# Kernel optimization log

Measured on AMD Instinct MI355X. Metric: run time of the kernel, lower is better.

## Reference

```python
import jax, jax.numpy as jnp
import numpy as np

B, D1, D2 = 131072, 40, 10   # batch, features, timesteps
T0, T1 = 120, 5              # template[1]
O0, O1 = 3, 1                # output_dim


def setup_inputs() -> dict:
    key = jax.random.key(0)
    ks = jax.random.split(key, 7)
    s = 0.1
    return {
        "x": jax.random.normal(ks[0], (B, D1, D2), dtype=jnp.float32),
        "W11": jax.random.normal(ks[1], (T0, D1), dtype=jnp.float32) * s,
        "fc2_w": jax.random.normal(ks[2], (T1, D2), dtype=jnp.float32) * s,  # nn.Linear(D2,T1) weight
        "bias1": jax.random.normal(ks[3], (T0, T1), dtype=jnp.float32) * s,
        "W12": jax.random.normal(ks[4], (O0, T0), dtype=jnp.float32) * s,
        "fc4_w": jax.random.normal(ks[5], (O1, T1), dtype=jnp.float32) * s,  # nn.Linear(T1,O1) weight
        "bias2": jax.random.normal(ks[6], (O0, O1), dtype=jnp.float32) * s,
    }


def reference(x, W11, fc2_w, bias1, W12, fc4_w, bias2):
    # item1[b] = W11 @ x[b]                 -> [B, T0, D2]
    item1 = jnp.einsum("td,bds->bts", W11, x)
    # item2[b] = fc2(item1[b]) + bias1      -> [B, T0, T1]; dropout is identity at eval
    item2 = jax.nn.relu(jnp.einsum("bts,us->btu", item1, fc2_w) + bias1)
    # item3[b] = W12 @ item2[b]             -> [B, O0, T1]
    item3 = jnp.einsum("ot,btu->bou", W12, item2)
    # item4[b] = fc4(item3[b]) + bias2      -> [B, O0, O1]
    item4 = jnp.einsum("bou,pu->bop", item3, fc4_w) + bias2
    # output_dim[1] == 1 -> squeeze last dim -> [B, O0]
    return item4[..., 0]
```

## Files before the change

### kernel.cpp

```cpp
#include <hip/hip_runtime.h>

#define NB  131072
#define ND1 40
#define ND2 10
#define NT0 120
#define NT1 5
#define NO0 3

#define NBW 32
#define XTILE (NBW * ND1 * ND2)
#define PK  40

typedef __attribute__((ext_vector_type(8))) short  short8;
typedef __attribute__((ext_vector_type(4))) float  f32x4;

static __device__ __forceinline__ unsigned short f2bf(float f) {
    union { float f; unsigned u; } v; v.f = f;
    unsigned r = v.u + 0x7FFFu + ((v.u >> 16) & 1u);
    return (unsigned short)(r >> 16);
}

__global__ __launch_bounds__(256, 2) void BL_36721970381090_kernel(
    const float* __restrict__ x,
    const float* __restrict__ W11,
    const float* __restrict__ fc2_w,
    const float* __restrict__ bias1,
    const float* __restrict__ W12,
    const float* __restrict__ fc4_w,
    const float* __restrict__ bias2,
    float* __restrict__ out)
{
    __shared__ __align__(16) unsigned short Ybf[NT1 * NBW * PK];
    __shared__ float biasL[128 * NT1];
    __shared__ float w12L[NO0 * 128];
    __shared__ float b2L[4];
    __shared__ float redL[4 * NO0 * NBW];

    const int tid = threadIdx.x;
    const int wg  = blockIdx.x;
    const int w   = tid >> 6;
    const int l   = tid & 63;
    const int lr  = l & 15;
    const int lg  = l >> 4;

    for (int i = tid; i < 128 * NT1; i += 256)
        biasL[i] = (i < NT0 * NT1) ? bias1[i] : 0.f;
    for (int i = tid; i < NO0 * 128; i += 256) {
        const int o = i >> 7, t = i & 127;
        w12L[i] = (t < NT0) ? W12[o * NT0 + t] : 0.f;
    }
    if (tid < NO0) b2L[tid] = bias2[tid];

    float fc4r[NT1];
#pragma unroll
    for (int u = 0; u < NT1; ++u) fc4r[u] = fc4_w[u];

    short8 afr[2][2];
#pragma unroll
    for (int mt = 0; mt < 2; ++mt) {
        const int t  = w * 32 + mt * 16 + lr;
        const int tc = t < NT0 ? t : NT0 - 1;
#pragma unroll
        for (int kk = 0; kk < 2; ++kk) {
            const int cb = kk * 32 + lg * 8;
            const int cc = cb <= 32 ? cb : 0;
            const float4* pw = (const float4*)(W11 + tc * ND1 + cc);
            const float4 w0 = pw[0], w1 = pw[1];
            const bool v = (t < NT0) && (cb <= 32);
            short8 f;
            f[0] = v ? (short)f2bf(w0.x) : (short)0;
            f[1] = v ? (short)f2bf(w0.y) : (short)0;
            f[2] = v ? (short)f2bf(w0.z) : (short)0;
            f[3] = v ? (short)f2bf(w0.w) : (short)0;
            f[4] = v ? (short)f2bf(w1.x) : (short)0;
            f[5] = v ? (short)f2bf(w1.y) : (short)0;
            f[6] = v ? (short)f2bf(w1.z) : (short)0;
            f[7] = v ? (short)f2bf(w1.w) : (short)0;
            afr[mt][kk] = f;
        }
    }

    {
        const float* gx = x + (size_t)wg * XTILE;
        unsigned* Yw = (unsigned*)Ybf;
#pragma unroll
        for (int rep = 0; rep < 3; ++rep) {
            const int  q   = rep * 256 + tid;
            const bool act = (rep < 2) || (tid < 128);
            if (act) {
                const int batch = q / 20;
                const int pair  = q - batch * 20;
                float4 xq[5];
                const float4* xr = (const float4*)(gx + q * 20);
#pragma unroll
                for (int i = 0; i < 5; ++i) xq[i] = xr[i];
                const float* xv = (const float*)xq;
#pragma unroll
                for (int u = 0; u < NT1; ++u) {
                    float a0 = 0.f, a1 = 0.f;
#pragma unroll
                    for (int s = 0; s < ND2; ++s) {
                        const float fw = fc2_w[u * ND2 + s];
                        a0 = fmaf(xv[s], fw, a0);
                        a1 = fmaf(xv[10 + s], fw, a1);
                    }
                    Yw[u * (NBW * PK / 2) + batch * (PK / 2) + pair] =
                        (unsigned)f2bf(a0) | ((unsigned)f2bf(a1) << 16);
                }
            }
        }
    }
    __syncthreads();

    float st[2][2][4];
#pragma unroll
    for (int mt = 0; mt < 2; ++mt)
#pragma unroll
        for (int nt = 0; nt < 2; ++nt)
#pragma unroll
            for (int r = 0; r < 4; ++r) st[mt][nt][r] = 0.f;

    const short8 zf = {0, 0, 0, 0, 0, 0, 0, 0};
#pragma unroll
    for (int u = 0; u < NT1; ++u) {
        float bv[2][4];
#pragma unroll
        for (int mt = 0; mt < 2; ++mt)
#pragma unroll
            for (int r = 0; r < 4; ++r)
                bv[mt][r] = biasL[(w * 32 + mt * 16 + lg * 4 + r) * NT1 + u];
        const unsigned short* Yu = &Ybf[u * (NBW * PK)];
#pragma unroll
        for (int nt = 0; nt < 2; ++nt) {
            const short8 b0 = *(const short8*)&Yu[(nt * 16 + lr) * PK + lg * 8];
            short8 b1 = zf;
            if (lg == 0) b1 = *(const short8*)&Yu[(nt * 16 + lr) * PK + 32];
#pragma unroll
            for (int mt = 0; mt < 2; ++mt) {
                f32x4 z = {0.f, 0.f, 0.f, 0.f};
                z = __builtin_amdgcn_mfma_f32_16x16x32_bf16(afr[mt][0], b0, z, 0, 0, 0);
                z = __builtin_amdgcn_mfma_f32_16x16x32_bf16(afr[mt][1], b1, z, 0, 0, 0);
#pragma unroll
                for (int r = 0; r < 4; ++r)
                    st[mt][nt][r] += fc4r[u] * fmaxf(z[r] + bv[mt][r], 0.f);
            }
        }
    }

    float po[2][NO0];
#pragma unroll
    for (int nt = 0; nt < 2; ++nt)
#pragma unroll
        for (int o = 0; o < NO0; ++o) {
            float a = 0.f;
#pragma unroll
            for (int mt = 0; mt < 2; ++mt)
#pragma unroll
                for (int r = 0; r < 4; ++r)
                    a = fmaf(w12L[o * 128 + (w * 32 + mt * 16 + lg * 4 + r)],
                             st[mt][nt][r], a);
            a += __shfl_xor(a, 16, 64);
            a += __shfl_xor(a, 32, 64);
            po[nt][o] = a;
        }
    if (l < 16) {
#pragma unroll
        for (int nt = 0; nt < 2; ++nt)
#pragma unroll
            for (int o = 0; o < NO0; ++o)
                redL[(w * NO0 + o) * NBW + nt * 16 + l] = po[nt][o];
    }
    __syncthreads();

    if (tid < NO0 * NBW) {
        const int o  = tid >> 5;
        const int bc = tid & 31;
        const float s = redL[(0 * NO0 + o) * NBW + bc]
                      + redL[(1 * NO0 + o) * NBW + bc]
                      + redL[(2 * NO0 + o) * NBW + bc]
                      + redL[(3 * NO0 + o) * NBW + bc]
                      + b2L[o];
        out[((size_t)wg * NBW + bc) * NO0 + o] = s;
    }
}

extern "C" void kernel_launch(void* const* d_in, const int* in_sizes, int n_in,
                              void* d_out, int out_size, void* d_ws, size_t ws_size,
                              hipStream_t stream) {
    const float* x      = (const float*)d_in[0];
    const float* W11    = (const float*)d_in[1];
    const float* fc2_w  = (const float*)d_in[2];
    const float* bias1  = (const float*)d_in[3];
    const float* W12    = (const float*)d_in[4];
    const float* fc4_w  = (const float*)d_in[5];
    const float* bias2  = (const float*)d_in[6];
    float* out = (float*)d_out;

    const int blocks = NB / NBW;
    BL_36721970381090_kernel<<<blocks, 256, 0, stream>>>(
        x, W11, fc2_w, bias1, W12, fc4_w, bias2, out);
}
```

Measured before the change: 50.71 us.

## Process two batch tiles per workgroup with software-pipelined load and compute

```diff
diff --git a/kernel.cpp b/kernel.cpp
--- a/kernel.cpp
+++ b/kernel.cpp
@@ -8,7 +8,7 @@
 #define NO0 3
 
 #define NBW 32
-#define XTILE (NBW * ND1 * ND2)
+#define XT  (NBW * ND1 * ND2)
 #define PK  40
 
 typedef __attribute__((ext_vector_type(8))) short  short8;
@@ -20,7 +20,7 @@
     return (unsigned short)(r >> 16);
 }
 
-__global__ __launch_bounds__(256, 2) void BL_36721970381090_kernel(
+__global__ __launch_bounds__(256) void BL_36721970381090_kernel(
     const float* __restrict__ x,
     const float* __restrict__ W11,
     const float* __restrict__ fc2_w,
@@ -30,11 +30,13 @@
     const float* __restrict__ bias2,
     float* __restrict__ out)
 {
-    __shared__ __align__(16) unsigned short Ybf[NT1 * NBW * PK];
+    __shared__ __align__(16) unsigned short YbfA[NT1 * NBW * PK];
+    __shared__ __align__(16) unsigned short YbfB[NT1 * NBW * PK];
     __shared__ float biasL[128 * NT1];
     __shared__ float w12L[NO0 * 128];
     __shared__ float b2L[4];
-    __shared__ float redL[4 * NO0 * NBW];
+    __shared__ float redLA[4 * NO0 * NBW];
+    __shared__ float redLB[4 * NO0 * NBW];
 
     const int tid = threadIdx.x;
     const int wg  = blockIdx.x;
@@ -80,21 +82,29 @@
         }
     }
 
-    {
-        const float* gx = x + (size_t)wg * XTILE;
-        unsigned* Yw = (unsigned*)Ybf;
+    const float* gxA = x + (size_t)(2 * wg) * XT;
+    const float* gxB = gxA + XT;
+
+    auto LOADX = [&](const float* gx, float4 (&xq)[3][5]) {
 #pragma unroll
         for (int rep = 0; rep < 3; ++rep) {
-            const int  q   = rep * 256 + tid;
-            const bool act = (rep < 2) || (tid < 128);
-            if (act) {
+            if (rep < 2 || tid < 128) {
+                const int q = rep * 256 + tid;
+                const float4* xr = (const float4*)(gx + q * 20);
+#pragma unroll
+                for (int i = 0; i < 5; ++i) xq[rep][i] = xr[i];
+            }
+        }
+    };
+    auto COMPY = [&](const float4 (&xq)[3][5], unsigned short* Yb) {
+        unsigned* Yw = (unsigned*)Yb;
+#pragma unroll
+        for (int rep = 0; rep < 3; ++rep) {
+            if (rep < 2 || tid < 128) {
+                const int q = rep * 256 + tid;
                 const int batch = q / 20;
                 const int pair  = q - batch * 20;
-                float4 xq[5];
-                const float4* xr = (const float4*)(gx + q * 20);
-#pragma unroll
-                for (int i = 0; i < 5; ++i) xq[i] = xr[i];
-                const float* xv = (const float*)xq;
+                const float* xv = (const float*)&xq[rep][0];
 #pragma unroll
                 for (int u = 0; u < NT1; ++u) {
                     float a0 = 0.f, a1 = 0.f;
@@ -109,79 +119,105 @@
                 }
             }
         }
-    }
-    __syncthreads();
-
-    float st[2][2][4];
-#pragma unroll
-    for (int mt = 0; mt < 2; ++mt)
+    };
+    auto PHASE2 = [&](const unsigned short* Yb, float (&po)[2][NO0]) {
+        float st[2][2][4];
+#pragma unroll
+        for (int mt = 0; mt < 2; ++mt)
+#pragma unroll
+            for (int nt = 0; nt < 2; ++nt)
+#pragma unroll
+                for (int r = 0; r < 4; ++r) st[mt][nt][r] = 0.f;
+        const short8 zf = {0, 0, 0, 0, 0, 0, 0, 0};
+#pragma unroll
+        for (int u = 0; u < NT1; ++u) {
+            float bv[2][4];
+#pragma unroll
+            for (int mt = 0; mt < 2; ++mt)
+#pragma unroll
+                for (int r = 0; r < 4; ++r)
+                    bv[mt][r] = biasL[(w * 32 + mt * 16 + lg * 4 + r) * NT1 + u];
+            const unsigned short* Yu = &Yb[u * (NBW * PK)];
+#pragma unroll
+            for (int nt = 0; nt < 2; ++nt) {
+                const short8 b0 = *(const short8*)&Yu[(nt * 16 + lr) * PK + lg * 8];
+                short8 b1 = zf;
+                if (lg == 0) b1 = *(const short8*)&Yu[(nt * 16 + lr) * PK + 32];
+#pragma unroll
+                for (int mt = 0; mt < 2; ++mt) {
+                    f32x4 z = {0.f, 0.f, 0.f, 0.f};
+                    z = __builtin_amdgcn_mfma_f32_16x16x32_bf16(afr[mt][0], b0, z, 0, 0, 0);
+                    z = __builtin_amdgcn_mfma_f32_16x16x32_bf16(afr[mt][1], b1, z, 0, 0, 0);
+#pragma unroll
+                    for (int r = 0; r < 4; ++r)
+                        st[mt][nt][r] += fc4r[u] * fmaxf(z[r] + bv[mt][r], 0.f);
+                }
+            }
+        }
 #pragma unroll
         for (int nt = 0; nt < 2; ++nt)
 #pragma unroll
-            for (int r = 0; r < 4; ++r) st[mt][nt][r] = 0.f;
-
-    const short8 zf = {0, 0, 0, 0, 0, 0, 0, 0};
-#pragma unroll
-    for (int u = 0; u < NT1; ++u) {
-        float bv[2][4];
-#pragma unroll
-        for (int mt = 0; mt < 2; ++mt)
-#pragma unroll
-            for (int r = 0; r < 4; ++r)
-                bv[mt][r] = biasL[(w * 32 + mt * 16 + lg * 4 + r) * NT1 + u];
-        const unsigned short* Yu = &Ybf[u * (NBW * PK)];
-#pragma unroll
-        for (int nt = 0; nt < 2; ++nt) {
-            const short8 b0 = *(const short8*)&Yu[(nt * 16 + lr) * PK + lg * 8];
-            short8 b1 = zf;
-            if (lg == 0) b1 = *(const short8*)&Yu[(nt * 16 + lr) * PK + 32];
-#pragma unroll
-            for (int mt = 0; mt < 2; ++mt) {
-                f32x4 z = {0.f, 0.f, 0.f, 0.f};
-                z = __builtin_amdgcn_mfma_f32_16x16x32_bf16(afr[mt][0], b0, z, 0, 0, 0);
-                z = __builtin_amdgcn_mfma_f32_16x16x32_bf16(afr[mt][1], b1, z, 0, 0, 0);
-#pragma unroll
-                for (int r = 0; r < 4; ++r)
-                    st[mt][nt][r] += fc4r[u] * fmaxf(z[r] + bv[mt][r], 0.f);
-            }
-        }
-    }
-
-    float po[2][NO0];
-#pragma unroll
-    for (int nt = 0; nt < 2; ++nt)
-#pragma unroll
-        for (int o = 0; o < NO0; ++o) {
-            float a = 0.f;
-#pragma unroll
-            for (int mt = 0; mt < 2; ++mt)
-#pragma unroll
-                for (int r = 0; r < 4; ++r)
-                    a = fmaf(w12L[o * 128 + (w * 32 + mt * 16 + lg * 4 + r)],
-                             st[mt][nt][r], a);
-            a += __shfl_xor(a, 16, 64);
-            a += __shfl_xor(a, 32, 64);
-            po[nt][o] = a;
-        }
-    if (l < 16) {
-#pragma unroll
-        for (int nt = 0; nt < 2; ++nt)
-#pragma unroll
-            for (int o = 0; o < NO0; ++o)
-                redL[(w * NO0 + o) * NBW + nt * 16 + l] = po[nt][o];
-    }
-    __syncthreads();
-
-    if (tid < NO0 * NBW) {
-        const int o  = tid >> 5;
-        const int bc = tid & 31;
-        const float s = redL[(0 * NO0 + o) * NBW + bc]
-                      + redL[(1 * NO0 + o) * NBW + bc]
-                      + redL[(2 * NO0 + o) * NBW + bc]
-                      + redL[(3 * NO0 + o) * NBW + bc]
-                      + b2L[o];
-        out[((size_t)wg * NBW + bc) * NO0 + o] = s;
-    }
+            for (int o = 0; o < NO0; ++o) {
+                float a = 0.f;
+#pragma unroll
+                for (int mt = 0; mt < 2; ++mt)
+#pragma unroll
+                    for (int r = 0; r < 4; ++r)
+                        a = fmaf(w12L[o * 128 + (w * 32 + mt * 16 + lg * 4 + r)],
+                                 st[mt][nt][r], a);
+                a += __shfl_xor(a, 16, 64);
+                a += __shfl_xor(a, 32, 64);
+                po[nt][o] = a;
+            }
+    };
+    auto REDW = [&](float* redL, const float (&po)[2][NO0]) {
+        if (l < 16) {
+#pragma unroll
+            for (int nt = 0; nt < 2; ++nt)
+#pragma unroll
+                for (int o = 0; o < NO0; ++o)
+                    redL[(w * NO0 + o) * NBW + nt * 16 + l] = po[nt][o];
+        }
+    };
+    auto OUTW = [&](const float* redL, int tileIdx) {
+        if (tid < NO0 * NBW) {
+            const int o  = tid >> 5;
+            const int bc = tid & 31;
+            const float s = redL[(0 * NO0 + o) * NBW + bc]
+                          + redL[(1 * NO0 + o) * NBW + bc]
+                          + redL[(2 * NO0 + o) * NBW + bc]
+                          + redL[(3 * NO0 + o) * NBW + bc]
+                          + b2L[o];
+            out[((size_t)(2 * wg + tileIdx) * NBW + bc) * NO0 + o] = s;
+        }
+    };
+
+    float4 xqA[3][5], xqB[3][5];
+
+    LOADX(gxA, xqA);
+    COMPY(xqA, YbfA);
+    LOADX(gxB, xqB);
+
+    asm volatile("s_waitcnt lgkmcnt(0)" ::: "memory");
+    __builtin_amdgcn_s_barrier();
+
+    float poA[2][NO0];
+    PHASE2(YbfA, poA);
+    COMPY(xqB, YbfB);
+    REDW(redLA, poA);
+
+    asm volatile("s_waitcnt lgkmcnt(0)" ::: "memory");
+    __builtin_amdgcn_s_barrier();
+
+    OUTW(redLA, 0);
+    float poB[2][NO0];
+    PHASE2(YbfB, poB);
+    REDW(redLB, poB);
+
+    asm volatile("s_waitcnt lgkmcnt(0)" ::: "memory");
+    __builtin_amdgcn_s_barrier();
+
+    OUTW(redLB, 1);
 }
 
 extern "C" void kernel_launch(void* const* d_in, const int* in_sizes, int n_in,
@@ -196,7 +232,7 @@
     const float* bias2  = (const float*)d_in[6];
     float* out = (float*)d_out;
 
-    const int blocks = NB / NBW;
+    const int blocks = NB / (2 * NBW);
     BL_36721970381090_kernel<<<blocks, 256, 0, stream>>>(
         x, W11, fc2_w, bias1, W12, fc4_w, bias2, out);
 }
```

New measurement: 69.49 us. 1.37x slower.
